# Optimization experiments

Measured on AMD Instinct MI355X. Metric: run time of the kernel, lower is better.

The kernel has to match this reference:

```python
import jax, jax.numpy as jnp
import numpy as np

BEV_RANGE = 32.0   # meters; traj xy normalized to [-1,1] by this half-range
NUM_HEADS = 8
EGO_FUT_TS = 8
EPS = 1e-5


def _ln(x, g, b):
    m = x.mean(-1, keepdims=True)
    v = ((x - m) ** 2).mean(-1, keepdims=True)
    return (x - m) / jnp.sqrt(v + EPS) * g + b


def _mha(q, k, v, wq, bq, wk, bk, wv, bv, wo, bo):
    B, Lq, D = q.shape
    Lk = k.shape[1]
    dh = D // NUM_HEADS
    qh = (q @ wq + bq).reshape(B, Lq, NUM_HEADS, dh).transpose(0, 2, 1, 3)
    kh = (k @ wk + bk).reshape(B, Lk, NUM_HEADS, dh).transpose(0, 2, 1, 3)
    vh = (v @ wv + bv).reshape(B, Lk, NUM_HEADS, dh).transpose(0, 2, 1, 3)
    a = jax.nn.softmax(jnp.einsum('bhqd,bhkd->bhqk', qh, kh) * (1.0 / float(np.sqrt(dh))), axis=-1)
    o = jnp.einsum('bhqk,bhkd->bhqd', a, vh).transpose(0, 2, 1, 3).reshape(B, Lq, D)
    return o @ wo + bo


def _grid_sample(value, grid):
    # value (B,C,H,W); grid (B,M,P,2) xy in [-1,1]; bilinear, zeros padding, align_corners=False
    B, C, H, W = value.shape
    x = (grid[..., 0] + 1.0) * (W * 0.5) - 0.5
    y = (grid[..., 1] + 1.0) * (H * 0.5) - 0.5
    x0 = jnp.floor(x)
    y0 = jnp.floor(y)
    bidx = jnp.arange(B)[:, None, None]

    def corner(xi, yi, w):
        valid = (xi >= 0) & (xi <= W - 1) & (yi >= 0) & (yi <= H - 1)
        xc = jnp.clip(xi, 0, W - 1).astype(jnp.int32)
        yc = jnp.clip(yi, 0, H - 1).astype(jnp.int32)
        v = value[bidx, :, yc, xc]  # advanced idx -> (B,M,P,C)
        return v * (w * valid)[..., None]

    return (corner(x0, y0, (x0 + 1 - x) * (y0 + 1 - y))
            + corner(x0 + 1, y0, (x - x0) * (y0 + 1 - y))
            + corner(x0, y0 + 1, (x0 + 1 - x) * (y - y0))
            + corner(x0 + 1, y0 + 1, (x - x0) * (y - y0)))


def _mish(x):
    return x * jnp.tanh(jax.nn.softplus(x))


def _forward(traj_feature, noisy_traj_points, bev_feature, agents_query, ego_query,
             time_embed, status_encoding,
             bev_value_w, bev_value_b, bev_attn_w, bev_attn_b, bev_out_w, bev_out_b,
             aq_wq, aq_bq, aq_wk, aq_bk, aq_wv, aq_bv, aq_wo, aq_bo,
             eq_wq, eq_bq, eq_wk, eq_bk, eq_wv, eq_bv, eq_wo, eq_bo,
             ffn_w1, ffn_b1, ffn_w2, ffn_b2,
             n1_g, n1_b, n2_g, n2_b, n3_g, n3_b,
             mod_w, mod_b,
             cls_w1, cls_b1, cls_ln1_g, cls_ln1_b, cls_w2, cls_b2, cls_ln2_g, cls_ln2_b, cls_w3, cls_b3,
             reg_w1, reg_b1, reg_w2, reg_b2, reg_w3, reg_b3):
    B, M, D = traj_feature.shape
    # --- GridSampleCrossBEVAttention ---
    value = jnp.einsum('bchw,cd->bdhw', bev_feature, bev_value_w) + bev_value_b[None, :, None, None]
    grid = noisy_traj_points / BEV_RANGE                    # (B,M,P,2) in [-1,1]
    sampled = _grid_sample(value, grid)                     # (B,M,P,D)
    pt_w = jax.nn.softmax(traj_feature @ bev_attn_w + bev_attn_b, axis=-1)  # (B,M,P)
    bev_out = jnp.einsum('bmpd,bmp->bmd', sampled, pt_w) @ bev_out_w + bev_out_b
    traj = traj_feature + bev_out
    # --- cross-agent attention + norm1 ---
    traj = _ln(traj + _mha(traj, agents_query, agents_query,
                           aq_wq, aq_bq, aq_wk, aq_bk, aq_wv, aq_bv, aq_wo, aq_bo), n1_g, n1_b)
    # --- cross-ego attention + norm2 ---
    traj = _ln(traj + _mha(traj, ego_query, ego_query,
                           eq_wq, eq_bq, eq_wk, eq_bk, eq_wv, eq_bv, eq_wo, eq_bo), n2_g, n2_b)
    # --- FFN + norm3 (note: no residual, matches source) ---
    traj = _ln(jax.nn.relu(traj @ ffn_w1 + ffn_b1) @ ffn_w2 + ffn_b2, n3_g, n3_b)
    # --- FiLM time modulation ---
    ss = _mish(time_embed) @ mod_w + mod_b                  # (B,1,2D)
    scale, shift = jnp.split(ss, 2, axis=-1)
    traj = traj * (1.0 + scale) + shift
    # --- task decoder: cls branch (linear_relu_ln x2 + Linear->1) ---
    h = _ln(jax.nn.relu(traj @ cls_w1 + cls_b1), cls_ln1_g, cls_ln1_b)
    h = _ln(jax.nn.relu(h @ cls_w2 + cls_b2), cls_ln2_g, cls_ln2_b)
    plan_cls = (h @ cls_w3 + cls_b3)[..., 0]                # (B,M)
    # --- task decoder: reg branch ---
    r = jax.nn.relu(traj @ reg_w1 + reg_b1)
    r = jax.nn.relu(r @ reg_w2 + reg_b2)
    r = (r @ reg_w3 + reg_b3).reshape(B, M, EGO_FUT_TS, 3)
    xy = r[..., :2] + noisy_traj_points
    heading = jnp.tanh(r[..., 2:3]) * np.pi
    poses_reg = jnp.concatenate([xy, heading], axis=-1)     # (B,M,T,3)
    return poses_reg, plan_cls


def setup_inputs() -> dict:
    key = jax.random.key(0)
    ks = iter(jax.random.split(key, 80))
    rn = lambda *s: jax.random.normal(next(ks), s, dtype=jnp.float32)
    w = lambda *s: rn(*s) * 0.05
    B, M, P, D, A, FF = 32, 20, 8, 256, 32, 1024
    inp = dict(
        traj_feature=rn(B, M, D),
        noisy_traj_points=rn(B, M, P, 2) * 8.0,
        bev_feature=rn(B, 256, 128, 128),
        agents_query=rn(B, A, D),
        ego_query=rn(B, 1, D),
        time_embed=rn(B, 1, D),
        status_encoding=rn(B, 1, D),
        bev_value_w=w(256, D), bev_value_b=jnp.zeros(D),
        bev_attn_w=w(D, P), bev_attn_b=jnp.zeros(P),
        bev_out_w=w(D, D), bev_out_b=jnp.zeros(D),
        aq_wq=w(D, D), aq_bq=jnp.zeros(D), aq_wk=w(D, D), aq_bk=jnp.zeros(D),
        aq_wv=w(D, D), aq_bv=jnp.zeros(D), aq_wo=w(D, D), aq_bo=jnp.zeros(D),
        eq_wq=w(D, D), eq_bq=jnp.zeros(D), eq_wk=w(D, D), eq_bk=jnp.zeros(D),
        eq_wv=w(D, D), eq_bv=jnp.zeros(D), eq_wo=w(D, D), eq_bo=jnp.zeros(D),
        ffn_w1=w(D, FF), ffn_b1=jnp.zeros(FF), ffn_w2=w(FF, D), ffn_b2=jnp.zeros(D),
        n1_g=jnp.ones(D), n1_b=jnp.zeros(D), n2_g=jnp.ones(D), n2_b=jnp.zeros(D),
        n3_g=jnp.ones(D), n3_b=jnp.zeros(D),
        mod_w=w(D, 2 * D), mod_b=jnp.zeros(2 * D),
        cls_w1=w(D, D), cls_b1=jnp.zeros(D), cls_ln1_g=jnp.ones(D), cls_ln1_b=jnp.zeros(D),
        cls_w2=w(D, D), cls_b2=jnp.zeros(D), cls_ln2_g=jnp.ones(D), cls_ln2_b=jnp.zeros(D),
        cls_w3=w(D, 1), cls_b3=jnp.full((1,), float(-np.log((1 - 0.01) / 0.01))),
        reg_w1=w(D, D), reg_b1=jnp.zeros(D), reg_w2=w(D, D), reg_b2=jnp.zeros(D),
        reg_w3=w(D, EGO_FUT_TS * 3), reg_b3=jnp.zeros(EGO_FUT_TS * 3),
        bev_spatial_shape=jnp.array([128, 128], dtype=jnp.int32),
    )
    return inp


def reference(traj_feature, noisy_traj_points, bev_feature, agents_query, ego_query,
              time_embed, status_encoding,
              bev_value_w, bev_value_b, bev_attn_w, bev_attn_b, bev_out_w, bev_out_b,
              aq_wq, aq_bq, aq_wk, aq_bk, aq_wv, aq_bv, aq_wo, aq_bo,
              eq_wq, eq_bq, eq_wk, eq_bk, eq_wv, eq_bv, eq_wo, eq_bo,
              ffn_w1, ffn_b1, ffn_w2, ffn_b2,
              n1_g, n1_b, n2_g, n2_b, n3_g, n3_b,
              mod_w, mod_b,
              cls_w1, cls_b1, cls_ln1_g, cls_ln1_b, cls_w2, cls_b2, cls_ln2_g, cls_ln2_b, cls_w3, cls_b3,
              reg_w1, reg_b1, reg_w2, reg_b2, reg_w3, reg_b3,
              bev_spatial_shape):
    # bev_spatial_shape is implied by bev_feature's static shape under jit
    return _forward(traj_feature, noisy_traj_points, bev_feature, agents_query, ego_query,
                    time_embed, status_encoding,
                    bev_value_w, bev_value_b, bev_attn_w, bev_attn_b, bev_out_w, bev_out_b,
                    aq_wq, aq_bq, aq_wk, aq_bk, aq_wv, aq_bv, aq_wo, aq_bo,
                    eq_wq, eq_bq, eq_wk, eq_bk, eq_wv, eq_bv, eq_wo, eq_bo,
                    ffn_w1, ffn_b1, ffn_w2, ffn_b2,
                    n1_g, n1_b, n2_g, n2_b, n3_g, n3_b,
                    mod_w, mod_b,
                    cls_w1, cls_b1, cls_ln1_g, cls_ln1_b, cls_w2, cls_b2, cls_ln2_g, cls_ln2_b, cls_w3, cls_b3,
                    reg_w1, reg_b1, reg_w2, reg_b2, reg_w3, reg_b3)
```

## Files before the change

### kernel.cpp

```cpp
#include <hip/hip_runtime.h>
#include <math.h>

constexpr int NB = 32;
constexpr int NM = 20;
constexpr int NP = 8;
constexpr int ND = 256;
constexpr int NA = 32;
constexpr int NFF = 1024;
constexpr int NH = 128, NW = 128;
constexpr int HW = NH * NW;

__device__ __forceinline__ float blk_sum(float v, float* s_red) {
    for (int off = 32; off > 0; off >>= 1) v += __shfl_down(v, off, 64);
    int tid = threadIdx.x;
    __syncthreads();
    if ((tid & 63) == 0) s_red[tid >> 6] = v;
    __syncthreads();
    return s_red[0] + s_red[1] + s_red[2] + s_red[3];
}

__device__ __forceinline__ float blk_ln(float x, const float* g, const float* bb, float* s_red) {
    int tid = threadIdx.x;
    float mean = blk_sum(x, s_red) * (1.0f / 256.0f);
    float xm = x - mean;
    float var = blk_sum(xm * xm, s_red) * (1.0f / 256.0f);
    return xm / sqrtf(var + 1e-5f) * g[tid] + bb[tid];
}

__global__ void gather_kernel(const float* __restrict__ traj, const float* __restrict__ noisy,
                              const float* __restrict__ bev, const float* __restrict__ attn_w,
                              const float* __restrict__ attn_b,
                              float* __restrict__ gw, float* __restrict__ wsumw) {
    int blk = blockIdx.x;
    int b = blk / NM, tid = threadIdx.x;
    __shared__ float s_traj[ND];
    __shared__ float s_ptw[NP];
    __shared__ float s_w[32];
    __shared__ int s_idx[32];

    s_traj[tid] = traj[(size_t)blk * ND + tid];
    __syncthreads();
    if (tid < NP) {
        float acc = attn_b[tid];
        for (int c = 0; c < ND; c++) acc += s_traj[c] * attn_w[c * NP + tid];
        s_ptw[tid] = acc;
    }
    __syncthreads();
    if (tid == 0) {
        float mx = s_ptw[0];
        for (int p = 1; p < NP; p++) mx = fmaxf(mx, s_ptw[p]);
        float e[NP], sum = 0.f;
        for (int p = 0; p < NP; p++) { e[p] = expf(s_ptw[p] - mx); sum += e[p]; }
        for (int p = 0; p < NP; p++) s_ptw[p] = e[p] / sum;
    }
    __syncthreads();
    if (tid < 32) {
        int p = tid >> 2, corner = tid & 3;
        float gx = noisy[((size_t)blk * NP + p) * 2 + 0] * (1.0f / 32.0f);
        float gy = noisy[((size_t)blk * NP + p) * 2 + 1] * (1.0f / 32.0f);
        float x = (gx + 1.0f) * (NW * 0.5f) - 0.5f;
        float y = (gy + 1.0f) * (NH * 0.5f) - 0.5f;
        float x0 = floorf(x), y0 = floorf(y);
        int dx = corner & 1, dy = corner >> 1;
        float wx = dx ? (x - x0) : (x0 + 1.0f - x);
        float wy = dy ? (y - y0) : (y0 + 1.0f - y);
        float xi = x0 + (float)dx, yi = y0 + (float)dy;
        bool valid = (xi >= 0.f) && (xi <= (float)(NW - 1)) && (yi >= 0.f) && (yi <= (float)(NH - 1));
        int xc = (int)fminf(fmaxf(xi, 0.f), (float)(NW - 1));
        int yc = (int)fminf(fmaxf(yi, 0.f), (float)(NH - 1));
        s_w[tid] = wx * wy * (valid ? 1.f : 0.f) * s_ptw[p];
        s_idx[tid] = yc * NW + xc;
    }
    __syncthreads();
    if (tid == 0) {
        float s = 0.f;
        for (int j = 0; j < 32; j++) s += s_w[j];
        wsumw[blk] = s;
    }
    const float* base = bev + (size_t)b * ND * HW + (size_t)tid * HW;
    float acc = 0.f;
    for (int j = 0; j < 32; j++) acc += s_w[j] * base[s_idx[j]];
    gw[(size_t)blk * ND + tid] = acc;
}

__global__ void kv_kernel(const float* __restrict__ agents,
                          const float* __restrict__ wk, const float* __restrict__ bk,
                          const float* __restrict__ wv, const float* __restrict__ bv,
                          float* __restrict__ K1, float* __restrict__ V1) {
    int blk = blockIdx.x, tid = threadIdx.x;
    __shared__ float s_row[ND];
    s_row[tid] = agents[(size_t)blk * ND + tid];
    __syncthreads();
    float ak = bk[tid], av = bv[tid];
    for (int c = 0; c < ND; c++) {
        float r = s_row[c];
        ak += r * wk[c * ND + tid];
        av += r * wv[c * ND + tid];
    }
    K1[(size_t)blk * ND + tid] = ak;
    V1[(size_t)blk * ND + tid] = av;
}

__global__ void perb_kernel(const float* __restrict__ ego,
                            const float* __restrict__ eq_wv, const float* __restrict__ eq_bv,
                            const float* __restrict__ eq_wo, const float* __restrict__ eq_bo,
                            const float* __restrict__ time_embed,
                            const float* __restrict__ mod_w, const float* __restrict__ mod_b,
                            float* __restrict__ u, float* __restrict__ ss) {
    int b = blockIdx.x, tid = threadIdx.x;
    __shared__ float s_a[ND], s_b[ND];
    s_a[tid] = ego[(size_t)b * ND + tid];
    __syncthreads();
    float v = eq_bv[tid];
    for (int c = 0; c < ND; c++) v += s_a[c] * eq_wv[c * ND + tid];
    s_b[tid] = v;
    __syncthreads();
    float o = eq_bo[tid];
    for (int c = 0; c < ND; c++) o += s_b[c] * eq_wo[c * ND + tid];
    u[(size_t)b * ND + tid] = o;

    float te = time_embed[(size_t)b * ND + tid];
    float sp = log1pf(expf(te));
    float me = te * tanhf(sp);
    __syncthreads();
    s_a[tid] = me;
    __syncthreads();
    for (int jj = 0; jj < 2; jj++) {
        int j = tid + jj * ND;
        float acc = mod_b[j];
        for (int c = 0; c < ND; c++) acc += s_a[c] * mod_w[(size_t)c * 2 * ND + j];
        ss[(size_t)b * 2 * ND + j] = acc;
    }
}

struct MegaW {
    const float *traj, *noisy;
    const float *bvw, *bvb, *bow, *bob;
    const float *wq, *bq, *wo, *bo;
    const float *n1g, *n1b, *n2g, *n2b;
    const float *fw1, *fb1, *fw2, *fb2, *n3g, *n3b;
    const float *cw1, *cb1, *cl1g, *cl1b, *cw2, *cb2, *cl2g, *cl2b, *cw3, *cb3;
    const float *rw1, *rb1, *rw2, *rb2, *rw3, *rb3;
};

__global__ void mega_kernel(const float* __restrict__ gw, const float* __restrict__ wsumw,
                            const float* __restrict__ K1, const float* __restrict__ V1,
                            const float* __restrict__ u, const float* __restrict__ ss,
                            MegaW W, float* __restrict__ out) {
    int blk = blockIdx.x;
    int b = blk / NM, tid = threadIdx.x;
    __shared__ float s_a[ND], s_b[ND], s_h[NFF], s_sc[ND], s_red[4];

    s_sc[tid] = gw[(size_t)blk * ND + tid];
    float wsw = wsumw[blk];
    __syncthreads();
    float acc = W.bvb[tid] * wsw;
    for (int c = 0; c < ND; c++) acc += s_sc[c] * W.bvw[c * ND + tid];
    s_b[tid] = acc;
    __syncthreads();
    acc = W.bob[tid] + W.traj[(size_t)blk * ND + tid];
    for (int c = 0; c < ND; c++) acc += s_b[c] * W.bow[c * ND + tid];
    s_a[tid] = acc;
    __syncthreads();
    acc = W.bq[tid];
    for (int c = 0; c < ND; c++) acc += s_a[c] * W.wq[c * ND + tid];
    s_b[tid] = acc;
    __syncthreads();
    int h = tid >> 5, kk = tid & 31;
    {
        const float* Krow = K1 + ((size_t)(b * NA + kk)) * ND + h * 32;
        float sc = 0.f;
        for (int j = 0; j < 32; j++) sc += s_b[h * 32 + j] * Krow[j];
        s_sc[tid] = sc * 0.17677669529663687f;
    }
    __syncthreads();
    {
        float mx = -1e30f;
        for (int j = 0; j < 32; j++) mx = fmaxf(mx, s_sc[h * 32 + j]);
        float den = 0.f;
        for (int j = 0; j < 32; j++) den += expf(s_sc[h * 32 + j] - mx);
        float p = expf(s_sc[tid] - mx) / den;
        __syncthreads();
        s_sc[tid] = p;
        __syncthreads();
    }
    {
        const float* Vb = V1 + (size_t)b * NA * ND;
        float o = 0.f;
        for (int k = 0; k < 32; k++) o += s_sc[h * 32 + k] * Vb[(size_t)k * ND + tid];
        __syncthreads();
        s_b[tid] = o;
        __syncthreads();
    }
    acc = W.bo[tid] + s_a[tid];
    for (int c = 0; c < ND; c++) acc += s_b[c] * W.wo[c * ND + tid];
    float t1 = blk_ln(acc, W.n1g, W.n1b, s_red);
    float t2 = blk_ln(t1 + u[(size_t)b * ND + tid], W.n2g, W.n2b, s_red);
    __syncthreads();
    s_a[tid] = t2;
    __syncthreads();
    for (int jj = 0; jj < 4; jj++) {
        int i = tid + jj * ND;
        float a2 = W.fb1[i];
        for (int c = 0; c < ND; c++) a2 += s_a[c] * W.fw1[(size_t)c * NFF + i];
        s_h[i] = fmaxf(a2, 0.f);
    }
    __syncthreads();
    acc = W.fb2[tid];
    for (int i = 0; i < NFF; i++) acc += s_h[i] * W.fw2[(size_t)i * ND + tid];
    float t3 = blk_ln(acc, W.n3g, W.n3b, s_red);
    float sc1 = ss[(size_t)b * 2 * ND + tid];
    float sh1 = ss[(size_t)b * 2 * ND + ND + tid];
    float tt = t3 * (1.f + sc1) + sh1;
    __syncthreads();
    s_a[tid] = tt;
    __syncthreads();
    acc = W.cb1[tid];
    for (int c = 0; c < ND; c++) acc += s_a[c] * W.cw1[c * ND + tid];
    float h1 = blk_ln(fmaxf(acc, 0.f), W.cl1g, W.cl1b, s_red);
    __syncthreads();
    s_b[tid] = h1;
    __syncthreads();
    acc = W.cb2[tid];
    for (int c = 0; c < ND; c++) acc += s_b[c] * W.cw2[c * ND + tid];
    float h2 = blk_ln(fmaxf(acc, 0.f), W.cl2g, W.cl2b, s_red);
    float pc = blk_sum(h2 * W.cw3[tid], s_red);
    if (tid == 0) out[(size_t)NB * NM * NP * 3 + blk] = pc + W.cb3[0];
    acc = W.rb1[tid];
    for (int c = 0; c < ND; c++) acc += s_a[c] * W.rw1[c * ND + tid];
    __syncthreads();
    s_b[tid] = fmaxf(acc, 0.f);
    __syncthreads();
    acc = W.rb2[tid];
    for (int c = 0; c < ND; c++) acc += s_b[c] * W.rw2[c * ND + tid];
    __syncthreads();
    s_b[tid] = fmaxf(acc, 0.f);
    __syncthreads();
    if (tid < 24) {
        float r3 = W.rb3[tid];
        for (int c = 0; c < ND; c++) r3 += s_b[c] * W.rw3[c * 24 + tid];
        int ts = tid / 3, k2 = tid % 3;
        float val;
        if (k2 < 2) val = r3 + W.noisy[((size_t)blk * NP + ts) * 2 + k2];
        else        val = tanhf(r3) * 3.14159265358979323846f;
        out[((size_t)blk * NP + ts) * 3 + k2] = val;
    }
}

extern "C" void kernel_launch(void* const* d_in, const int* in_sizes, int n_in,
                              void* d_out, int out_size, void* d_ws, size_t ws_size,
                              hipStream_t stream) {
    const float* traj   = (const float*)d_in[0];
    const float* noisy  = (const float*)d_in[1];
    const float* bev    = (const float*)d_in[2];
    const float* agents = (const float*)d_in[3];
    const float* ego    = (const float*)d_in[4];
    const float* temb   = (const float*)d_in[5];
    const float* bvw = (const float*)d_in[7];
    const float* bvb = (const float*)d_in[8];
    const float* baw = (const float*)d_in[9];
    const float* bab = (const float*)d_in[10];
    const float* bow = (const float*)d_in[11];
    const float* bob = (const float*)d_in[12];
    const float* aq_wq = (const float*)d_in[13];
    const float* aq_bq = (const float*)d_in[14];
    const float* aq_wk = (const float*)d_in[15];
    const float* aq_bk = (const float*)d_in[16];
    const float* aq_wv = (const float*)d_in[17];
    const float* aq_bv = (const float*)d_in[18];
    const float* aq_wo = (const float*)d_in[19];
    const float* aq_bo = (const float*)d_in[20];
    const float* eq_wv = (const float*)d_in[25];
    const float* eq_bv = (const float*)d_in[26];
    const float* eq_wo = (const float*)d_in[27];
    const float* eq_bo = (const float*)d_in[28];
    const float* fw1 = (const float*)d_in[29];
    const float* fb1 = (const float*)d_in[30];
    const float* fw2 = (const float*)d_in[31];
    const float* fb2 = (const float*)d_in[32];
    const float* n1g = (const float*)d_in[33];
    const float* n1b = (const float*)d_in[34];
    const float* n2g = (const float*)d_in[35];
    const float* n2b = (const float*)d_in[36];
    const float* n3g = (const float*)d_in[37];
    const float* n3b = (const float*)d_in[38];
    const float* modw = (const float*)d_in[39];
    const float* modb = (const float*)d_in[40];
    const float* cw1 = (const float*)d_in[41];
    const float* cb1 = (const float*)d_in[42];
    const float* cl1g = (const float*)d_in[43];
    const float* cl1b = (const float*)d_in[44];
    const float* cw2 = (const float*)d_in[45];
    const float* cb2 = (const float*)d_in[46];
    const float* cl2g = (const float*)d_in[47];
    const float* cl2b = (const float*)d_in[48];
    const float* cw3 = (const float*)d_in[49];
    const float* cb3 = (const float*)d_in[50];
    const float* rw1 = (const float*)d_in[51];
    const float* rb1 = (const float*)d_in[52];
    const float* rw2 = (const float*)d_in[53];
    const float* rb2 = (const float*)d_in[54];
    const float* rw3 = (const float*)d_in[55];
    const float* rb3 = (const float*)d_in[56];

    float* ws = (float*)d_ws;
    float* gw    = ws;
    float* wsumw = ws + 163840;
    float* K1    = ws + 164480;
    float* V1    = ws + 426624;
    float* u     = ws + 688768;
    float* ssb   = ws + 696960;

    gather_kernel<<<dim3(NB * NM), dim3(256), 0, stream>>>(traj, noisy, bev, baw, bab, gw, wsumw);
    kv_kernel<<<dim3(NB * NA), dim3(256), 0, stream>>>(agents, aq_wk, aq_bk, aq_wv, aq_bv, K1, V1);
    perb_kernel<<<dim3(NB), dim3(256), 0, stream>>>(ego, eq_wv, eq_bv, eq_wo, eq_bo, temb, modw, modb, u, ssb);

    MegaW W;
    W.traj = traj; W.noisy = noisy;
    W.bvw = bvw; W.bvb = bvb; W.bow = bow; W.bob = bob;
    W.wq = aq_wq; W.bq = aq_bq; W.wo = aq_wo; W.bo = aq_bo;
    W.n1g = n1g; W.n1b = n1b; W.n2g = n2g; W.n2b = n2b;
    W.fw1 = fw1; W.fb1 = fb1; W.fw2 = fw2; W.fb2 = fb2; W.n3g = n3g; W.n3b = n3b;
    W.cw1 = cw1; W.cb1 = cb1; W.cl1g = cl1g; W.cl1b = cl1b;
    W.cw2 = cw2; W.cb2 = cb2; W.cl2g = cl2g; W.cl2b = cl2b; W.cw3 = cw3; W.cb3 = cb3;
    W.rw1 = rw1; W.rb1 = rb1; W.rw2 = rw2; W.rb2 = rb2; W.rw3 = rw3; W.rb3 = rb3;

    mega_kernel<<<dim3(NB * NM), dim3(256), 0, stream>>>(gw, wsumw, K1, V1, u, ssb, W, (float*)d_out);
}
```

Baseline: 954.9 us.

## Pack weights to bf16 with 4-row interleave and vectorize GEMV loops

Adds a pack kernel that converts the dense weight matrices to bf16 each call, interleaving groups of four input rows so each thread loads a uint2 holding four weights. The mega and kv kernels then read these packed weights with float4 shared-memory activations, which halves weight bandwidth and cuts load instruction count. The kv kernel also processes two agents per block to reuse weight loads, and the gather loop gets two accumulators. This lowers weight precision to bf16, which may affect accuracy, and adds a per-call conversion pass.

```diff
diff --git a/kernel.cpp b/kernel.cpp
--- a/kernel.cpp
+++ b/kernel.cpp
@@ -9,6 +9,82 @@
 constexpr int NFF = 1024;
 constexpr int NH = 128, NW = 128;
 constexpr int HW = NH * NW;
+
+constexpr int PK_BVW = 0;
+constexpr int PK_BOW = 65536;
+constexpr int PK_WQ  = 131072;
+constexpr int PK_WO  = 196608;
+constexpr int PK_CW1 = 262144;
+constexpr int PK_CW2 = 327680;
+constexpr int PK_RW1 = 393216;
+constexpr int PK_RW2 = 458752;
+constexpr int PK_WK  = 524288;
+constexpr int PK_WV  = 589824;
+constexpr int PK_FW1 = 655360;
+constexpr int PK_FW2 = 917504;
+constexpr int PK_TOTAL = 1179648;
+
+constexpr int WS_GW   = 0;
+constexpr int WS_WSUM = 163840;
+constexpr int WS_K1   = 164480;
+constexpr int WS_V1   = 426624;
+constexpr int WS_U    = 688768;
+constexpr int WS_SS   = 696960;
+constexpr int WS_PACK = 720896;
+
+__device__ __forceinline__ void dec2(unsigned u, float& f0, float& f1) {
+    union { unsigned x; float f; } a, b;
+    a.x = u << 16;
+    b.x = u & 0xffff0000u;
+    f0 = a.f; f1 = b.f;
+}
+
+__device__ __forceinline__ float fma4(float4 a, uint2 w, float acc) {
+    float w0, w1, w2, w3;
+    dec2(w.x, w0, w1);
+    dec2(w.y, w2, w3);
+    acc += a.x * w0;
+    acc += a.y * w1;
+    acc += a.z * w2;
+    acc += a.w * w3;
+    return acc;
+}
+
+__device__ __forceinline__ float gemm256(const uint2* __restrict__ wp, const float* __restrict__ sa,
+                                         int tid, float acc) {
+    const float4* a4 = (const float4*)sa;
+    #pragma unroll 8
+    for (int c4 = 0; c4 < 64; ++c4) {
+        float4 a = a4[c4];
+        uint2 w = wp[(c4 << 8) + tid];
+        acc = fma4(a, w, acc);
+    }
+    return acc;
+}
+
+struct PackArgs {
+    const float* src[12];
+    int log2N[12];
+    int elems[12];
+    int dstoff[12];
+};
+
+__global__ void pack_kernel(PackArgs pa, unsigned short* __restrict__ dst) {
+    int e = blockIdx.x * 256 + threadIdx.x;
+    int seg = 0;
+    while (seg < 12 && e >= pa.elems[seg]) { e -= pa.elems[seg]; seg++; }
+    if (seg >= 12) return;
+    int lg = pa.log2N[seg];
+    int N = 1 << lg;
+    int c = e >> lg;
+    int n = e & (N - 1);
+    float v = pa.src[seg][e];
+    union { float f; unsigned u; } uu; uu.f = v;
+    unsigned x = uu.u;
+    unsigned r = (x + 0x7fff + ((x >> 16) & 1)) >> 16;
+    int idx = (((c >> 2) << lg) + n) * 4 + (c & 3);
+    dst[pa.dstoff[seg] + idx] = (unsigned short)r;
+}
 
 __device__ __forceinline__ float blk_sum(float v, float* s_red) {
     for (int off = 32; off > 0; off >>= 1) v += __shfl_down(v, off, 64);
@@ -78,27 +154,40 @@
         wsumw[blk] = s;
     }
     const float* base = bev + (size_t)b * ND * HW + (size_t)tid * HW;
-    float acc = 0.f;
-    for (int j = 0; j < 32; j++) acc += s_w[j] * base[s_idx[j]];
-    gw[(size_t)blk * ND + tid] = acc;
+    float acc0 = 0.f, acc1 = 0.f;
+    #pragma unroll
+    for (int j = 0; j < 32; j += 2) {
+        acc0 += s_w[j]     * base[s_idx[j]];
+        acc1 += s_w[j + 1] * base[s_idx[j + 1]];
+    }
+    gw[(size_t)blk * ND + tid] = acc0 + acc1;
 }
 
 __global__ void kv_kernel(const float* __restrict__ agents,
-                          const float* __restrict__ wk, const float* __restrict__ bk,
-                          const float* __restrict__ wv, const float* __restrict__ bv,
+                          const uint2* __restrict__ wkp, const float* __restrict__ bk,
+                          const uint2* __restrict__ wvp, const float* __restrict__ bv,
                           float* __restrict__ K1, float* __restrict__ V1) {
     int blk = blockIdx.x, tid = threadIdx.x;
-    __shared__ float s_row[ND];
-    s_row[tid] = agents[(size_t)blk * ND + tid];
-    __syncthreads();
-    float ak = bk[tid], av = bv[tid];
-    for (int c = 0; c < ND; c++) {
-        float r = s_row[c];
-        ak += r * wk[c * ND + tid];
-        av += r * wv[c * ND + tid];
-    }
-    K1[(size_t)blk * ND + tid] = ak;
-    V1[(size_t)blk * ND + tid] = av;
+    int a0 = blk * 2;
+    __shared__ __align__(16) float s0[ND], s1[ND];
+    s0[tid] = agents[(size_t)a0 * ND + tid];
+    s1[tid] = agents[(size_t)(a0 + 1) * ND + tid];
+    __syncthreads();
+    float k0 = bk[tid], k1 = k0, v0 = bv[tid], v1 = v0;
+    const float4* p0 = (const float4*)s0;
+    const float4* p1 = (const float4*)s1;
+    #pragma unroll 8
+    for (int c4 = 0; c4 < 64; ++c4) {
+        float4 a0f = p0[c4], a1f = p1[c4];
+        uint2 wk = wkp[(c4 << 8) + tid];
+        uint2 wv = wvp[(c4 << 8) + tid];
+        k0 = fma4(a0f, wk, k0); k1 = fma4(a1f, wk, k1);
+        v0 = fma4(a0f, wv, v0); v1 = fma4(a1f, wv, v1);
+    }
+    K1[(size_t)a0 * ND + tid] = k0;
+    K1[(size_t)(a0 + 1) * ND + tid] = k1;
+    V1[(size_t)a0 * ND + tid] = v0;
+    V1[(size_t)(a0 + 1) * ND + tid] = v1;
 }
 
 __global__ void perb_kernel(const float* __restrict__ ego,
@@ -135,35 +224,42 @@
 
 struct MegaW {
     const float *traj, *noisy;
-    const float *bvw, *bvb, *bow, *bob;
-    const float *wq, *bq, *wo, *bo;
+    const float *bvb, *bob, *bq, *bo;
     const float *n1g, *n1b, *n2g, *n2b;
-    const float *fw1, *fb1, *fw2, *fb2, *n3g, *n3b;
-    const float *cw1, *cb1, *cl1g, *cl1b, *cw2, *cb2, *cl2g, *cl2b, *cw3, *cb3;
-    const float *rw1, *rb1, *rw2, *rb2, *rw3, *rb3;
+    const float *fb1, *fb2, *n3g, *n3b;
+    const float *cb1, *cl1g, *cl1b, *cb2, *cl2g, *cl2b, *cw3, *cb3;
+    const float *rb1, *rb2, *rw3, *rb3;
 };
 
 __global__ void mega_kernel(const float* __restrict__ gw, const float* __restrict__ wsumw,
                             const float* __restrict__ K1, const float* __restrict__ V1,
                             const float* __restrict__ u, const float* __restrict__ ss,
+                            const uint2* __restrict__ bvwp, const uint2* __restrict__ bowp,
+                            const uint2* __restrict__ wqp, const uint2* __restrict__ wop,
+                            const uint2* __restrict__ fw1p, const uint2* __restrict__ fw2p,
+                            const uint2* __restrict__ cw1p, const uint2* __restrict__ cw2p,
+                            const uint2* __restrict__ rw1p, const uint2* __restrict__ rw2p,
                             MegaW W, float* __restrict__ out) {
     int blk = blockIdx.x;
     int b = blk / NM, tid = threadIdx.x;
-    __shared__ float s_a[ND], s_b[ND], s_h[NFF], s_sc[ND], s_red[4];
+    __shared__ __align__(16) float s_a[ND];
+    __shared__ __align__(16) float s_b[ND];
+    __shared__ __align__(16) float s_h[NFF];
+    __shared__ __align__(16) float s_sc[ND];
+    __shared__ float s_red[4];
 
     s_sc[tid] = gw[(size_t)blk * ND + tid];
     float wsw = wsumw[blk];
     __syncthreads();
-    float acc = W.bvb[tid] * wsw;
-    for (int c = 0; c < ND; c++) acc += s_sc[c] * W.bvw[c * ND + tid];
+    float acc = gemm256(bvwp, s_sc, tid, W.bvb[tid] * wsw);
+    __syncthreads();
     s_b[tid] = acc;
     __syncthreads();
-    acc = W.bob[tid] + W.traj[(size_t)blk * ND + tid];
-    for (int c = 0; c < ND; c++) acc += s_b[c] * W.bow[c * ND + tid];
+    acc = gemm256(bowp, s_b, tid, W.bob[tid] + W.traj[(size_t)blk * ND + tid]);
     s_a[tid] = acc;
     __syncthreads();
-    acc = W.bq[tid];
-    for (int c = 0; c < ND; c++) acc += s_a[c] * W.wq[c * ND + tid];
+    acc = gemm256(wqp, s_a, tid, W.bq[tid]);
+    __syncthreads();
     s_b[tid] = acc;
     __syncthreads();
     int h = tid >> 5, kk = tid & 31;
@@ -192,22 +288,37 @@
         s_b[tid] = o;
         __syncthreads();
     }
-    acc = W.bo[tid] + s_a[tid];
-    for (int c = 0; c < ND; c++) acc += s_b[c] * W.wo[c * ND + tid];
+    acc = gemm256(wop, s_b, tid, W.bo[tid] + s_a[tid]);
     float t1 = blk_ln(acc, W.n1g, W.n1b, s_red);
     float t2 = blk_ln(t1 + u[(size_t)b * ND + tid], W.n2g, W.n2b, s_red);
     __syncthreads();
     s_a[tid] = t2;
     __syncthreads();
-    for (int jj = 0; jj < 4; jj++) {
-        int i = tid + jj * ND;
-        float a2 = W.fb1[i];
-        for (int c = 0; c < ND; c++) a2 += s_a[c] * W.fw1[(size_t)c * NFF + i];
-        s_h[i] = fmaxf(a2, 0.f);
-    }
-    __syncthreads();
-    acc = W.fb2[tid];
-    for (int i = 0; i < NFF; i++) acc += s_h[i] * W.fw2[(size_t)i * ND + tid];
+    {
+        float f0 = W.fb1[tid], f1 = W.fb1[tid + 256], f2 = W.fb1[tid + 512], f3 = W.fb1[tid + 768];
+        const float4* a4 = (const float4*)s_a;
+        #pragma unroll 4
+        for (int c4 = 0; c4 < 64; ++c4) {
+            float4 a = a4[c4];
+            f0 = fma4(a, fw1p[(c4 << 10) + tid], f0);
+            f1 = fma4(a, fw1p[(c4 << 10) + 256 + tid], f1);
+            f2 = fma4(a, fw1p[(c4 << 10) + 512 + tid], f2);
+            f3 = fma4(a, fw1p[(c4 << 10) + 768 + tid], f3);
+        }
+        s_h[tid] = fmaxf(f0, 0.f);
+        s_h[tid + 256] = fmaxf(f1, 0.f);
+        s_h[tid + 512] = fmaxf(f2, 0.f);
+        s_h[tid + 768] = fmaxf(f3, 0.f);
+    }
+    __syncthreads();
+    {
+        acc = W.fb2[tid];
+        const float4* h4 = (const float4*)s_h;
+        #pragma unroll 8
+        for (int c4 = 0; c4 < 256; ++c4) {
+            acc = fma4(h4[c4], fw2p[(c4 << 8) + tid], acc);
+        }
+    }
     float t3 = blk_ln(acc, W.n3g, W.n3b, s_red);
     float sc1 = ss[(size_t)b * 2 * ND + tid];
     float sh1 = ss[(size_t)b * 2 * ND + ND + tid];
@@ -215,24 +326,20 @@
     __syncthreads();
     s_a[tid] = tt;
     __syncthreads();
-    acc = W.cb1[tid];
-    for (int c = 0; c < ND; c++) acc += s_a[c] * W.cw1[c * ND + tid];
+    acc = gemm256(cw1p, s_a, tid, W.cb1[tid]);
     float h1 = blk_ln(fmaxf(acc, 0.f), W.cl1g, W.cl1b, s_red);
     __syncthreads();
     s_b[tid] = h1;
     __syncthreads();
-    acc = W.cb2[tid];
-    for (int c = 0; c < ND; c++) acc += s_b[c] * W.cw2[c * ND + tid];
+    acc = gemm256(cw2p, s_b, tid, W.cb2[tid]);
     float h2 = blk_ln(fmaxf(acc, 0.f), W.cl2g, W.cl2b, s_red);
     float pc = blk_sum(h2 * W.cw3[tid], s_red);
     if (tid == 0) out[(size_t)NB * NM * NP * 3 + blk] = pc + W.cb3[0];
-    acc = W.rb1[tid];
-    for (int c = 0; c < ND; c++) acc += s_a[c] * W.rw1[c * ND + tid];
+    acc = gemm256(rw1p, s_a, tid, W.rb1[tid]);
     __syncthreads();
     s_b[tid] = fmaxf(acc, 0.f);
     __syncthreads();
-    acc = W.rb2[tid];
-    for (int c = 0; c < ND; c++) acc += s_b[c] * W.rw2[c * ND + tid];
+    acc = gemm256(rw2p, s_b, tid, W.rb2[tid]);
     __syncthreads();
     s_b[tid] = fmaxf(acc, 0.f);
     __syncthreads();
@@ -304,26 +411,41 @@
     const float* rb3 = (const float*)d_in[56];
 
     float* ws = (float*)d_ws;
-    float* gw    = ws;
-    float* wsumw = ws + 163840;
-    float* K1    = ws + 164480;
-    float* V1    = ws + 426624;
-    float* u     = ws + 688768;
-    float* ssb   = ws + 696960;
+    float* gw    = ws + WS_GW;
+    float* wsumw = ws + WS_WSUM;
+    float* K1    = ws + WS_K1;
+    float* V1    = ws + WS_V1;
+    float* u     = ws + WS_U;
+    float* ssb   = ws + WS_SS;
+    unsigned short* pk = (unsigned short*)(ws + WS_PACK);
+
+    PackArgs pa;
+    const float* srcs[12] = {bvw, bow, aq_wq, aq_wo, cw1, cw2, rw1, rw2, aq_wk, aq_wv, fw1, fw2};
+    int lg[12]   = {8, 8, 8, 8, 8, 8, 8, 8, 8, 8, 10, 8};
+    int el[12]   = {65536, 65536, 65536, 65536, 65536, 65536, 65536, 65536, 65536, 65536, 262144, 262144};
+    int off[12]  = {PK_BVW, PK_BOW, PK_WQ, PK_WO, PK_CW1, PK_CW2, PK_RW1, PK_RW2, PK_WK, PK_WV, PK_FW1, PK_FW2};
+    for (int i = 0; i < 12; i++) { pa.src[i] = srcs[i]; pa.log2N[i] = lg[i]; pa.elems[i] = el[i]; pa.dstoff[i] = off[i]; }
+    pack_kernel<<<dim3(PK_TOTAL / 256), dim3(256), 0, stream>>>(pa, pk);
 
     gather_kernel<<<dim3(NB * NM), dim3(256), 0, stream>>>(traj, noisy, bev, baw, bab, gw, wsumw);
-    kv_kernel<<<dim3(NB * NA), dim3(256), 0, stream>>>(agents, aq_wk, aq_bk, aq_wv, aq_bv, K1, V1);
+    kv_kernel<<<dim3(NB * NA / 2), dim3(256), 0, stream>>>(agents,
+        (const uint2*)(pk + PK_WK), aq_bk, (const uint2*)(pk + PK_WV), aq_bv, K1, V1);
     perb_kernel<<<dim3(NB), dim3(256), 0, stream>>>(ego, eq_wv, eq_bv, eq_wo, eq_bo, temb, modw, modb, u, ssb);
 
     MegaW W;
     W.traj = traj; W.noisy = noisy;
-    W.bvw = bvw; W.bvb = bvb; W.bow = bow; W.bob = bob;
-    W.wq = aq_wq; W.bq = aq_bq; W.wo = aq_wo; W.bo = aq_bo;
+    W.bvb = bvb; W.bob = bob; W.bq = aq_bq; W.bo = aq_bo;
     W.n1g = n1g; W.n1b = n1b; W.n2g = n2g; W.n2b = n2b;
-    W.fw1 = fw1; W.fb1 = fb1; W.fw2 = fw2; W.fb2 = fb2; W.n3g = n3g; W.n3b = n3b;
-    W.cw1 = cw1; W.cb1 = cb1; W.cl1g = cl1g; W.cl1b = cl1b;
-    W.cw2 = cw2; W.cb2 = cb2; W.cl2g = cl2g; W.cl2b = cl2b; W.cw3 = cw3; W.cb3 = cb3;
-    W.rw1 = rw1; W.rb1 = rb1; W.rw2 = rw2; W.rb2 = rb2; W.rw3 = rw3; W.rb3 = rb3;
-
-    mega_kernel<<<dim3(NB * NM), dim3(256), 0, stream>>>(gw, wsumw, K1, V1, u, ssb, W, (float*)d_out);
-}
+    W.fb1 = fb1; W.fb2 = fb2; W.n3g = n3g; W.n3b = n3b;
+    W.cb1 = cb1; W.cl1g = cl1g; W.cl1b = cl1b;
+    W.cb2 = cb2; W.cl2g = cl2g; W.cl2b = cl2b; W.cw3 = cw3; W.cb3 = cb3;
+    W.rb1 = rb1; W.rb2 = rb2; W.rw3 = rw3; W.rb3 = rb3;
+
+    mega_kernel<<<dim3(NB * NM), dim3(256), 0, stream>>>(gw, wsumw, K1, V1, u, ssb,
+        (const uint2*)(pk + PK_BVW), (const uint2*)(pk + PK_BOW),
+        (const uint2*)(pk + PK_WQ),  (const uint2*)(pk + PK_WO),
+        (const uint2*)(pk + PK_FW1), (const uint2*)(pk + PK_FW2),
+        (const uint2*)(pk + PK_CW1), (const uint2*)(pk + PK_CW2),
+        (const uint2*)(pk + PK_RW1), (const uint2*)(pk + PK_RW2),
+        W, (float*)d_out);
+}
```

New measurement: 897.3 us. -6.0%, faster.
